# Performance work log

Hardware: AMD Instinct MI355X
Metric: run time of the kernel (lower is better)

The kernel has to match this reference:

```python
import jax, jax.numpy as jnp
import numpy as np
from jax.ops import segment_sum, segment_max

N_NODES = 100000
N_EDGES = 1600000


def _glorot(key, shape):
    fan_in, fan_out = shape[0], shape[-1]
    lim = np.sqrt(6.0 / (fan_in + fan_out))
    return jax.random.uniform(key, shape, jnp.float32, -lim, lim)


def setup_inputs() -> dict:
    key = jax.random.key(0)
    ks = jax.random.split(key, 12)
    x = jax.random.normal(ks[0], (N_NODES, 7), jnp.float32)
    edge_index = jax.random.randint(ks[1], (2, N_EDGES), 0, N_NODES, jnp.int64)
    return {
        "x": x,
        "edge_index": edge_index,
        # GCNConv(7, 32)
        "W1": _glorot(ks[2], (7, 32)), "b1": jnp.zeros((32,), jnp.float32),
        # GATConv(32, 64), heads=1
        "W2": _glorot(ks[3], (32, 64)), "a_src2": _glorot(ks[4], (64, 1))[:, 0],
        "a_dst2": _glorot(ks[5], (64, 1))[:, 0], "b2": jnp.zeros((64,), jnp.float32),
        # GCNConv(64, 128)
        "W3": _glorot(ks[6], (64, 128)), "b3": jnp.zeros((128,), jnp.float32),
        # GATConv(128, 2), heads=1
        "W4": _glorot(ks[7], (128, 2)), "a_src4": _glorot(ks[8], (2, 1))[:, 0],
        "a_dst4": _glorot(ks[9], (2, 1))[:, 0], "b4": jnp.zeros((2,), jnp.float32),
    }


def _gcn_conv(x, src, dst, W, b):
    # x' = W x; symmetric normalization with self-loops already in (src, dst)
    h = x @ W
    deg = segment_sum(jnp.ones_like(dst, dtype=h.dtype), dst, num_segments=N_NODES)
    dinv = jnp.where(deg > 0, jax.lax.rsqrt(deg), 0.0)
    norm = dinv[src] * dinv[dst]            # [E]
    msg = norm[:, None] * h[src]            # [E, C]
    return segment_sum(msg, dst, num_segments=N_NODES) + b


def _gat_conv(x, src, dst, W, a_src, a_dst, b, slope=0.2):
    h = x @ W                               # [N, C]
    alpha_src = h @ a_src                   # [N]
    alpha_dst = h @ a_dst                   # [N]
    e = alpha_src[src] + alpha_dst[dst]     # [E]
    e = jnp.where(e > 0, e, slope * e)      # leaky_relu
    # numerically-stable softmax over edges grouped by destination node
    m = segment_max(e, dst, num_segments=N_NODES)
    ex = jnp.exp(e - m[dst])
    denom = segment_sum(ex, dst, num_segments=N_NODES)
    w = ex / (denom[dst] + 1e-16)           # [E]
    out = segment_sum(w[:, None] * h[src], dst, num_segments=N_NODES)
    return out + b


def reference(x, edge_index, W1, b1, W2, a_src2, a_dst2, b2, W3, b3, W4, a_src4, a_dst4, b4):
    # add self-loops once (PyG does it per layer; identical edge set each time)
    loop = jnp.arange(N_NODES, dtype=edge_index.dtype)
    src = jnp.concatenate([edge_index[0], loop])
    dst = jnp.concatenate([edge_index[1], loop])

    h = _gcn_conv(x, src, dst, W1, b1)
    h = jax.nn.relu(h)
    h = _gat_conv(h, src, dst, W2, a_src2, a_dst2, b2)
    h = jax.nn.relu(h)
    h = _gcn_conv(h, src, dst, W3, b3)
    h = jax.nn.relu(h)
    h = _gat_conv(h, src, dst, W4, a_src4, a_dst4, b4)
    return jax.nn.log_softmax(h, axis=1)
```

## Files before the change

kernel.cpp:

```cpp
#include <hip/hip_runtime.h>
#include <hip/hip_bf16.h>

#define NN 100000
#define NE 1600000
#define NT (NN + NE)
#define NBKT 256
#define BSZ 391
#define BCAP 10240

typedef unsigned int u32;
typedef unsigned short u16;

static __device__ __forceinline__ int clampN(int s) {
    return ((unsigned)s < (unsigned)NN) ? s : 0;
}
static __device__ __forceinline__ int ld_src(const int* ei, int is32, int e) {
    return is32 ? ei[e] : ei[2 * e];
}
static __device__ __forceinline__ int ld_dst(const int* ei, int is32, int e) {
    return is32 ? ei[NE + e] : ei[2 * NE + 2 * e];
}
static __device__ __forceinline__ float2 b2x2(u32 u) {
    float2 r;
    r.x = __uint_as_float((u & 0xffffu) << 16);
    r.y = __uint_as_float(u & 0xffff0000u);
    return r;
}
static __device__ __forceinline__ u16 f2bs(float f) {
    union { __hip_bfloat16 b; u16 u; } cv;
    cv.b = __float2bfloat16(f);
    return cv.u;
}
static __device__ __forceinline__ u32 pack2(float x, float y) {
    return ((u32)f2bs(y) << 16) | (u32)f2bs(x);
}
static __device__ __forceinline__ float lrelu_c(float e) {
    e = (e > 0.f) ? e : 0.2f * e;
    return fminf(e, 60.f);
}

#define FMA4(acc, s, v) { acc.x += (s)*(v).x; acc.y += (s)*(v).y; \
                          acc.z += (s)*(v).z; acc.w += (s)*(v).w; }


__global__ void __launch_bounds__(256) k_init(const float* __restrict__ W2,
                                              const float* __restrict__ a2s,
                                              const float* __restrict__ a2d,
                                              const int* __restrict__ ei,
                                              float* __restrict__ va2,
                                              float* __restrict__ vd2,
                                              int* __restrict__ flag,
                                              int* __restrict__ gcur) {
    if (blockIdx.x == 0) {
        if (threadIdx.x == 0) flag[0] = 0;
        __syncthreads();
        int nz = 0;
        for (int i = threadIdx.x; i < 4096; i += 256) nz |= ei[2 * i + 1];
        if (nz) atomicOr(flag, 1);
        if (threadIdx.x < NBKT) gcur[threadIdx.x] = 0;
    } else if (threadIdx.x < 64) {
        int t = threadIdx.x;
        if (t < 32) {
            float a = 0.f;
            for (int c = 0; c < 64; c++) a += W2[t * 64 + c] * a2s[c];
            va2[t] = a;
        } else {
            int k = t - 32;
            float a = 0.f;
            for (int c = 0; c < 64; c++) a += W2[k * 64 + c] * a2d[c];
            vd2[k] = a;
        }
    }
}


__global__ void __launch_bounds__(256) k_binA(const int* __restrict__ ei,
                                              const int* __restrict__ flag,
                                              int* __restrict__ gcur,
                                              u32* __restrict__ staging) {
    __shared__ int hist[NBKT];
    __shared__ int gbase[NBKT];
    __shared__ int cnt2[NBKT];
    int tid = threadIdx.x;
    if (tid < NBKT) hist[tid] = 0;
    __syncthreads();

    int base = blockIdx.x * 4096;
    int is32 = flag[0];
    int d[16], s[16];
    #pragma unroll
    for (int i = 0; i < 16; i++) {
        int e = base + i * 256 + tid;
        d[i] = -1;
        if (e < NE) {
            int dd = ld_dst(ei, is32, e);
            if ((unsigned)dd < (unsigned)NN) { d[i] = dd; s[i] = clampN(ld_src(ei, is32, e)); }
        } else if (e < NT) {
            d[i] = e - NE; s[i] = e - NE;
        }
        if (d[i] >= 0) atomicAdd(&hist[d[i] / BSZ], 1);
    }
    __syncthreads();
    if (tid < NBKT) {
        int c = hist[tid];
        gbase[tid] = c ? atomicAdd(&gcur[tid], c) : 0;
        cnt2[tid] = 0;
    }
    __syncthreads();
    #pragma unroll
    for (int i = 0; i < 16; i++) {
        if (d[i] >= 0) {
            int b = d[i] / BSZ;
            int pos = gbase[b] + atomicAdd(&cnt2[b], 1);
            if (pos < BCAP)
                staging[(size_t)b * BCAP + pos] =
                    ((unsigned)(d[i] - b * BSZ) << 17) | (unsigned)s[i];
        }
    }
}

__global__ void __launch_bounds__(256) k_histscan(const u32* __restrict__ staging,
                                                  const int* __restrict__ gcur,
                                                  const float* __restrict__ x,
                                                  u32* __restrict__ xpb,
                                                  int* __restrict__ rowptr,
                                                  int* __restrict__ deg,
                                                  int* __restrict__ part) {
    __shared__ int h[512];
    __shared__ int sm[256];
    int b = blockIdx.x, tid = threadIdx.x;
    h[tid] = 0; h[tid + 256] = 0;
    __syncthreads();
    int cnt = min(gcur[b], BCAP);
    const u32* st = staging + (size_t)b * BCAP;
    for (int i = tid; i < cnt; i += 256)
        atomicAdd(&h[st[i] >> 17], 1);
    __syncthreads();
    int h0 = h[2 * tid], h1 = h[2 * tid + 1];
    int pair = h0 + h1;
    sm[tid] = pair;
    __syncthreads();
    for (int off = 1; off < 256; off <<= 1) {
        int t = (tid >= off) ? sm[tid - off] : 0;
        __syncthreads();
        sm[tid] += t;
        __syncthreads();
    }
    int excl = sm[tid] - pair;
    int g0 = b * BSZ + 2 * tid;
    if (2 * tid < BSZ && g0 < NN) { rowptr[g0] = excl; deg[g0] = h0; }
    int g1 = g0 + 1;
    if (2 * tid + 1 < BSZ && g1 < NN) { rowptr[g1] = excl + h0; deg[g1] = h1; }
    if (tid == 255) part[b] = sm[255];

    for (int i = b * 256 + tid; i < NN * 4; i += NBKT * 256) {
        int n = i >> 2, c2 = i & 3;
        float f0 = x[n * 7 + 2 * c2];
        float f1 = (2 * c2 + 1 < 7) ? x[n * 7 + 2 * c2 + 1] : 0.f;
        xpb[i] = pack2(f0, f1);
    }
}

__global__ void __launch_bounds__(256) k_scat(const u32* __restrict__ staging,
                                              const int* __restrict__ gcur,
                                              const int* __restrict__ part,
                                              int* __restrict__ rowptr,
                                              const int* __restrict__ deg,
                                              float* __restrict__ dinv,
                                              int* __restrict__ col) {
    __shared__ int sm[256];
    __shared__ int cur[BSZ];
    int b = blockIdx.x, tid = threadIdx.x;
    int v = part[tid];
    sm[tid] = v;
    __syncthreads();
    for (int off = 1; off < 256; off <<= 1) {
        int t = (tid >= off) ? sm[tid - off] : 0;
        __syncthreads();
        sm[tid] += t;
        __syncthreads();
    }
    int pb = (b > 0) ? sm[b - 1] : 0;
    if (b == 0 && tid == 0) rowptr[NN] = NT;
    for (int l = tid; l < BSZ; l += 256) {
        int g = b * BSZ + l;
        if (g < NN) {
            int r = rowptr[g] + pb;
            rowptr[g] = r;
            cur[l] = r;
            int d = deg[g];
            dinv[g] = rsqrtf((float)(d > 0 ? d : 1));
        } else cur[l] = 0;
    }
    __syncthreads();
    int cnt = min(gcur[b], BCAP);
    const u32* st = staging + (size_t)b * BCAP;
    for (int i = tid; i < cnt; i += 256) {
        u32 w = st[i];
        int l = w >> 17;
        int s = w & 0x1FFFF;
        int p = atomicAdd(&cur[l], 1);
        if ((unsigned)p < (unsigned)NT) col[p] = s;
    }
}


__global__ void __launch_bounds__(256) k_l1(const u32* __restrict__ xpb,
                                            const int* __restrict__ rowptr,
                                            const int* __restrict__ col,
                                            const float* __restrict__ dinv,
                                            const float* __restrict__ W1,
                                            const float* __restrict__ b1,
                                            const float* __restrict__ va2,
                                            const float* __restrict__ vd2,
                                            u32* __restrict__ O1b,
                                            float* __restrict__ as_,
                                            float* __restrict__ ad_) {
    __shared__ float sW1[7 * 32];
    __shared__ float sb1[32], sva[32], svd[32];
    __shared__ float sT1[64 * 8];
    if (threadIdx.x < 224) sW1[threadIdx.x] = W1[threadIdx.x];
    else {
        int c = threadIdx.x - 224;
        sb1[c] = b1[c]; sva[c] = va2[c]; svd[c] = vd2[c];
    }
    __syncthreads();

    int node_l = threadIdx.x >> 2;
    int lane = threadIdx.x & 3;
    int slot = lane >> 1;
    int ck = lane & 1;
    int n = blockIdx.x * 64 + node_l;
    if (n >= NN) return;
    {
        int beg = rowptr[n], end = rowptr[n + 1];
        float a0 = 0.f, a1 = 0.f, a2 = 0.f, a3 = 0.f;
        #pragma unroll 2
        for (int e = beg + slot; e < end; e += 2) {
            int s = clampN(col[e]);
            float w = dinv[s];
            uint2 u = *(const uint2*)(xpb + (size_t)s * 4 + ck * 2);
            float2 f0 = b2x2(u.x), f1 = b2x2(u.y);
            a0 += w * f0.x; a1 += w * f0.y; a2 += w * f1.x; a3 += w * f1.y;
        }
        a0 += __shfl_xor(a0, 2, 4); a1 += __shfl_xor(a1, 2, 4);
        a2 += __shfl_xor(a2, 2, 4); a3 += __shfl_xor(a3, 2, 4);
        if (slot == 0) {
            float dn = dinv[n];
            float4 o = {a0 * dn, a1 * dn, a2 * dn, a3 * dn};
            *(float4*)&sT1[node_l * 8 + ck * 4] = o;
        }
    }
    __builtin_amdgcn_wave_barrier();
    int c8 = lane * 8;
    float4 aA = {0,0,0,0}, aB = {0,0,0,0};
    #pragma unroll
    for (int k = 0; k < 7; k++) {
        float t = sT1[node_l * 8 + k];
        float4 wva = *(const float4*)&sW1[k * 32 + c8];
        float4 wvb = *(const float4*)&sW1[k * 32 + c8 + 4];
        FMA4(aA, t, wva);
        FMA4(aB, t, wvb);
    }
    float o0 = fmaxf(aA.x + sb1[c8], 0.f);
    float o1 = fmaxf(aA.y + sb1[c8 + 1], 0.f);
    float o2 = fmaxf(aA.z + sb1[c8 + 2], 0.f);
    float o3 = fmaxf(aA.w + sb1[c8 + 3], 0.f);
    float o4 = fmaxf(aB.x + sb1[c8 + 4], 0.f);
    float o5 = fmaxf(aB.y + sb1[c8 + 5], 0.f);
    float o6 = fmaxf(aB.z + sb1[c8 + 6], 0.f);
    float o7 = fmaxf(aB.w + sb1[c8 + 7], 0.f);
    uint4 pk = {pack2(o0, o1), pack2(o2, o3), pack2(o4, o5), pack2(o6, o7)};
    *(uint4*)(O1b + (size_t)n * 16 + lane * 4) = pk;
    float vs = o0 * sva[c8] + o1 * sva[c8 + 1] + o2 * sva[c8 + 2] + o3 * sva[c8 + 3]
             + o4 * sva[c8 + 4] + o5 * sva[c8 + 5] + o6 * sva[c8 + 6] + o7 * sva[c8 + 7];
    float vd = o0 * svd[c8] + o1 * svd[c8 + 1] + o2 * svd[c8 + 2] + o3 * svd[c8 + 3]
             + o4 * svd[c8 + 4] + o5 * svd[c8 + 5] + o6 * svd[c8 + 6] + o7 * svd[c8 + 7];
    vs += __shfl_xor(vs, 1, 4); vs += __shfl_xor(vs, 2, 4);
    vd += __shfl_xor(vd, 1, 4); vd += __shfl_xor(vd, 2, 4);
    if (lane == 0) { as_[n] = vs; ad_[n] = vd; }
}


__global__ void __launch_bounds__(256) k_l2(const u32* __restrict__ O1b,
                                            const float* __restrict__ as_,
                                            const float* __restrict__ ad_,
                                            const int* __restrict__ rowptr,
                                            const int* __restrict__ col,
                                            const float* __restrict__ W2,
                                            const float* __restrict__ b2,
                                            const float* __restrict__ dinv,
                                            u32* __restrict__ O2b) {
    __shared__ float sW2[32 * 64];
    __shared__ float sT2[32 * 36];
    __shared__ float sb2[64];
    {
        const float4* g = (const float4*)W2;
        float4* s4 = (float4*)sW2;
        s4[threadIdx.x] = g[threadIdx.x];
        s4[threadIdx.x + 256] = g[threadIdx.x + 256];
    }
    if (threadIdx.x < 64) sb2[threadIdx.x] = b2[threadIdx.x];
    __syncthreads();

    int node_l = threadIdx.x >> 3;
    int l8 = threadIdx.x & 7;
    int slot = l8 >> 2;
    int ck = l8 & 3;
    int n = blockIdx.x * 32 + node_l;
    {
        int beg = rowptr[n], end = rowptr[n + 1];
        float adn = ad_[n];
        float den = 0.f;
        float a0=0.f,a1=0.f,a2=0.f,a3=0.f,a4=0.f,a5=0.f,a6=0.f,a7=0.f;
        #pragma unroll 2
        for (int e = beg + slot; e < end; e += 2) {
            int s = clampN(col[e]);
            float p = __expf(lrelu_c(as_[s] + adn));
            den += p;
            uint4 w = *(const uint4*)(O1b + (size_t)s * 16 + ck * 4);
            float2 f0 = b2x2(w.x), f1 = b2x2(w.y), f2 = b2x2(w.z), f3 = b2x2(w.w);
            a0 += p * f0.x; a1 += p * f0.y; a2 += p * f1.x; a3 += p * f1.y;
            a4 += p * f2.x; a5 += p * f2.y; a6 += p * f3.x; a7 += p * f3.y;
        }
        den += __shfl_xor(den, 4, 8);
        a0 += __shfl_xor(a0, 4, 8); a1 += __shfl_xor(a1, 4, 8);
        a2 += __shfl_xor(a2, 4, 8); a3 += __shfl_xor(a3, 4, 8);
        a4 += __shfl_xor(a4, 4, 8); a5 += __shfl_xor(a5, 4, 8);
        a6 += __shfl_xor(a6, 4, 8); a7 += __shfl_xor(a7, 4, 8);
        if (slot == 0) {
            float inv = 1.0f / (den + 1e-16f);
            float4 oA = {a0 * inv, a1 * inv, a2 * inv, a3 * inv};
            float4 oB = {a4 * inv, a5 * inv, a6 * inv, a7 * inv};
            float* dst = &sT2[node_l * 36 + ck * 8];
            *(float4*)dst = oA;
            *(float4*)(dst + 4) = oB;
        }
    }
    __builtin_amdgcn_wave_barrier();

    int grp = threadIdx.x >> 4;
    int l = threadIdx.x & 15;
    int c4 = l * 4;
    int lbase = grp * 2;

    float4 acc0 = {0,0,0,0}, acc1 = {0,0,0,0};
    #pragma unroll
    for (int k4 = 0; k4 < 8; k4++) {
        float4 t0 = *(const float4*)&sT2[(lbase + 0) * 36 + 4 * k4];
        float4 t1 = *(const float4*)&sT2[(lbase + 1) * 36 + 4 * k4];
        #pragma unroll
        for (int j = 0; j < 4; j++) {
            float4 wv = *(const float4*)&sW2[(4 * k4 + j) * 64 + c4];
            FMA4(acc0, ((const float*)&t0)[j], wv);
            FMA4(acc1, ((const float*)&t1)[j], wv);
        }
    }
    float4 bb = *(const float4*)&sb2[c4];
    int n0 = blockIdx.x * 32 + lbase;
    float d0 = dinv[n0], d1 = dinv[n0 + 1];
    {
        float o0 = fmaxf(acc0.x + bb.x, 0.f) * d0;
        float o1 = fmaxf(acc0.y + bb.y, 0.f) * d0;
        float o2 = fmaxf(acc0.z + bb.z, 0.f) * d0;
        float o3 = fmaxf(acc0.w + bb.w, 0.f) * d0;
        uint2 pk = {pack2(o0, o1), pack2(o2, o3)};
        *(uint2*)(O2b + (size_t)n0 * 32 + l * 2) = pk;
    }
    {
        float o0 = fmaxf(acc1.x + bb.x, 0.f) * d1;
        float o1 = fmaxf(acc1.y + bb.y, 0.f) * d1;
        float o2 = fmaxf(acc1.z + bb.z, 0.f) * d1;
        float o3 = fmaxf(acc1.w + bb.w, 0.f) * d1;
        uint2 pk = {pack2(o0, o1), pack2(o2, o3)};
        *(uint2*)(O2b + (size_t)(n0 + 1) * 32 + l * 2) = pk;
    }
}


__global__ void __launch_bounds__(512) k_l3(const u32* __restrict__ O2b,
                                            const int* __restrict__ rowptr,
                                            const int* __restrict__ col,
                                            const float* __restrict__ dinv,
                                            const float* __restrict__ W3,
                                            const float* __restrict__ b3,
                                            const float* __restrict__ W4,
                                            const float* __restrict__ av4s,
                                            const float* __restrict__ av4d,
                                            float4* __restrict__ h4as,
                                            float* __restrict__ ad_) {
    __shared__ float sW3[64 * 128];
    __shared__ float sT3[64 * 68];
    __shared__ float sW4[128 * 2];
    __shared__ float sb3[128];

    {
        const float4* g = (const float4*)W3;
        float4* s4 = (float4*)sW3;
        #pragma unroll
        for (int i = 0; i < 4; i++) s4[threadIdx.x + 512 * i] = g[threadIdx.x + 512 * i];
    }
    if (threadIdx.x < 128) {
        sb3[threadIdx.x] = b3[threadIdx.x];
        sW4[2 * threadIdx.x] = W4[2 * threadIdx.x];
        sW4[2 * threadIdx.x + 1] = W4[2 * threadIdx.x + 1];
    }
    __syncthreads();

    int w = threadIdx.x >> 6;
    int l = threadIdx.x & 63;
    int g8 = l >> 3;
    int row = w * 8 + g8;
    int n = blockIdx.x * 64 + row;
    if (n >= NN) return;

    {
        int slot = (l >> 2) & 1;
        int ck = l & 3;
        int beg = rowptr[n], end = rowptr[n + 1];
        float2 ac[8];
        #pragma unroll
        for (int i = 0; i < 8; i++) { ac[i].x = 0.f; ac[i].y = 0.f; }
        #pragma unroll 2
        for (int e = beg + slot; e < end; e += 2) {
            int s = clampN(col[e]);
            const uint4* rp = (const uint4*)(O2b + (size_t)s * 32 + ck * 8);
            uint4 wa = rp[0];
            uint4 wb = rp[1];
            float2 f;
            f = b2x2(wa.x); ac[0].x += f.x; ac[0].y += f.y;
            f = b2x2(wa.y); ac[1].x += f.x; ac[1].y += f.y;
            f = b2x2(wa.z); ac[2].x += f.x; ac[2].y += f.y;
            f = b2x2(wa.w); ac[3].x += f.x; ac[3].y += f.y;
            f = b2x2(wb.x); ac[4].x += f.x; ac[4].y += f.y;
            f = b2x2(wb.y); ac[5].x += f.x; ac[5].y += f.y;
            f = b2x2(wb.z); ac[6].x += f.x; ac[6].y += f.y;
            f = b2x2(wb.w); ac[7].x += f.x; ac[7].y += f.y;
        }
        #pragma unroll
        for (int i = 0; i < 8; i++) {
            ac[i].x += __shfl_xor(ac[i].x, 4, 8);
            ac[i].y += __shfl_xor(ac[i].y, 4, 8);
        }
        if (slot == 0) {
            float dn = dinv[n];
            float* dst = &sT3[row * 68 + ck * 16];
            float4 o0 = {ac[0].x * dn, ac[0].y * dn, ac[1].x * dn, ac[1].y * dn};
            float4 o1 = {ac[2].x * dn, ac[2].y * dn, ac[3].x * dn, ac[3].y * dn};
            float4 o2 = {ac[4].x * dn, ac[4].y * dn, ac[5].x * dn, ac[5].y * dn};
            float4 o3 = {ac[6].x * dn, ac[6].y * dn, ac[7].x * dn, ac[7].y * dn};
            *(float4*)&dst[0]  = o0;
            *(float4*)&dst[4]  = o1;
            *(float4*)&dst[8]  = o2;
            *(float4*)&dst[12] = o3;
        }
    }
    __builtin_amdgcn_wave_barrier();

    int cl = l & 7;
    const float* trow = &sT3[row * 68];
    float4 acc0 = {0,0,0,0}, acc1 = {0,0,0,0}, acc2 = {0,0,0,0}, acc3 = {0,0,0,0};
    #pragma unroll 4
    for (int k4 = 0; k4 < 16; k4++) {
        float4 t4 = *(const float4*)&trow[k4 * 4];
        #pragma unroll
        for (int j = 0; j < 4; j++) {
            float tj = ((const float*)&t4)[j];
            const float* wr = &sW3[(k4 * 4 + j) * 128 + 4 * cl];
            float4 w0 = *(const float4*)&wr[0];
            float4 w1 = *(const float4*)&wr[32];
            float4 w2 = *(const float4*)&wr[64];
            float4 w3v = *(const float4*)&wr[96];
            FMA4(acc0, tj, w0);
            FMA4(acc1, tj, w1);
            FMA4(acc2, tj, w2);
            FMA4(acc3, tj, w3v);
        }
    }

    float av4s0 = av4s[0], av4s1 = av4s[1];
    float av4d0 = av4d[0], av4d1 = av4d[1];
    float p0 = 0.f, p1 = 0.f;
    #pragma unroll
    for (int q = 0; q < 4; q++) {
        float4 a = (q == 0) ? acc0 : (q == 1) ? acc1 : (q == 2) ? acc2 : acc3;
        int c = 4 * cl + 32 * q;
        float4 bb = *(const float4*)&sb3[c];
        a.x = fmaxf(a.x + bb.x, 0.f);
        a.y = fmaxf(a.y + bb.y, 0.f);
        a.z = fmaxf(a.z + bb.z, 0.f);
        a.w = fmaxf(a.w + bb.w, 0.f);
        p0 += a.x * sW4[2 * c]     + a.y * sW4[2 * (c + 1)]
            + a.z * sW4[2 * (c + 2)] + a.w * sW4[2 * (c + 3)];
        p1 += a.x * sW4[2 * c + 1]     + a.y * sW4[2 * (c + 1) + 1]
            + a.z * sW4[2 * (c + 2) + 1] + a.w * sW4[2 * (c + 3) + 1];
    }
    p0 += __shfl_xor(p0, 1, 8); p0 += __shfl_xor(p0, 2, 8); p0 += __shfl_xor(p0, 4, 8);
    p1 += __shfl_xor(p1, 1, 8); p1 += __shfl_xor(p1, 2, 8); p1 += __shfl_xor(p1, 4, 8);
    if (cl == 0) {
        float asv = p0 * av4s0 + p1 * av4s1;
        float4 pk = {p0, p1, asv, 0.f};
        h4as[n] = pk;
        ad_[n] = p0 * av4d0 + p1 * av4d1;
    }
}


__global__ void k_final(const float4* __restrict__ h4as,
                        const float* __restrict__ ad_, const int* __restrict__ rowptr,
                        const int* __restrict__ col, const float* __restrict__ b,
                        float* __restrict__ out) {
    int gid = blockIdx.x * 256 + threadIdx.x;
    int n = gid >> 2;
    if (n >= NN) return;
    int lsub = gid & 3;
    int beg = rowptr[n], end = rowptr[n + 1];
    float adn = ad_[n];
    float den = 0.f, a0 = 0.f, a1 = 0.f;
    for (int e = beg + lsub; e < end; e += 4) {
        int s = clampN(col[e]);
        float4 h = h4as[s];
        float p = __expf(lrelu_c(h.z + adn));
        den += p;
        a0 += p * h.x;
        a1 += p * h.y;
    }
    den += __shfl_xor(den, 1, 4); den += __shfl_xor(den, 2, 4);
    a0  += __shfl_xor(a0, 1, 4);  a0  += __shfl_xor(a0, 2, 4);
    a1  += __shfl_xor(a1, 1, 4);  a1  += __shfl_xor(a1, 2, 4);
    if (lsub == 0) {
        float inv = 1.0f / (den + 1e-16f);
        float v0 = a0 * inv + b[0];
        float v1 = a1 * inv + b[1];
        float mx = fmaxf(v0, v1);
        float lse = mx + logf(__expf(v0 - mx) + __expf(v1 - mx));
        float2 o = {v0 - lse, v1 - lse};
        *(float2*)(out + n * 2) = o;
    }
}

__global__ void k_sentinel(float* __restrict__ out, float v) {
    int i = blockIdx.x * 256 + threadIdx.x;
    if (i < NN * 2) out[i] = v;
}


extern "C" void kernel_launch(void* const* d_in, const int* in_sizes, int n_in,
                              void* d_out, int out_size, void* d_ws, size_t ws_size,
                              hipStream_t stream) {
    const float* x    = (const float*)d_in[0];
    const int* ei     = (const int*)d_in[1];
    const float* W1   = (const float*)d_in[2];
    const float* b1   = (const float*)d_in[3];
    const float* W2   = (const float*)d_in[4];
    const float* a2s  = (const float*)d_in[5];
    const float* a2d  = (const float*)d_in[6];
    const float* b2   = (const float*)d_in[7];
    const float* W3   = (const float*)d_in[8];
    const float* b3   = (const float*)d_in[9];
    const float* W4   = (const float*)d_in[10];
    const float* a4s  = (const float*)d_in[11];
    const float* a4d  = (const float*)d_in[12];
    const float* b4   = (const float*)d_in[13];
    float* out = (float*)d_out;

    char* base = (char*)d_ws;
    size_t off = 0;
    auto alloc = [&](size_t bytes) {
        char* q = base + off;
        off += (bytes + 255) & ~(size_t)255;
        return q;
    };
    u32* xpb     = (u32*)alloc((size_t)NN * 4 * 4);
    u32* O1b     = (u32*)alloc((size_t)NN * 16 * 4);
    u32* O2b     = (u32*)alloc((size_t)NN * 32 * 4);
    u32* staging = (u32*)alloc((size_t)NBKT * BCAP * 4);
    int* col     = (int*)alloc((size_t)NT * 4);
    int* rowptr  = (int*)alloc((size_t)(NN + 1) * 4);
    int* deg     = (int*)alloc((size_t)NN * 4);
    float* dinv  = (float*)alloc((size_t)NN * 4);
    float* as_   = (float*)alloc((size_t)NN * 4);
    float* ad_   = (float*)alloc((size_t)NN * 4);
    float4* h4as = (float4*)alloc((size_t)NN * 16);
    int* part    = (int*)alloc(512 * 4);
    int* flag    = (int*)alloc(256);
    int* gcur    = (int*)alloc(NBKT * 4);
    float* va2   = (float*)alloc(32 * 4);
    float* vd2   = (float*)alloc(32 * 4);

    float code = 0.f;
    if (off > ws_size)            code = 1000.f + (float)(ws_size >> 20);
    else if (n_in != 14)          code = 2000.f + 10.f * (float)n_in;
    else if (out_size != NN * 2)  code = 3400.f;
    if (code != 0.f) {
        k_sentinel<<<(NN * 2 + 255) / 256, 256, 0, stream>>>(out, code);
        return;
    }

    const int NTILE = (NT + 4095) / 4096;

    k_init<<<2, 256, 0, stream>>>(W2, a2s, a2d, ei, va2, vd2, flag, gcur);
    k_binA<<<NTILE, 256, 0, stream>>>(ei, flag, gcur, staging);
    k_histscan<<<NBKT, 256, 0, stream>>>(staging, gcur, x, xpb, rowptr, deg, part);
    k_scat<<<NBKT, 256, 0, stream>>>(staging, gcur, part, rowptr, deg, dinv, col);

    k_l1<<<(NN + 63) / 64, 256, 0, stream>>>(xpb, rowptr, col, dinv,
                                             W1, b1, va2, vd2, O1b, as_, ad_);
    k_l2<<<NN / 32, 256, 0, stream>>>(O1b, as_, ad_, rowptr, col,
                                      W2, b2, dinv, O2b);
    k_l3<<<(NN + 63) / 64, 512, 0, stream>>>(O2b, rowptr, col, dinv,
                                             W3, b3, W4, a4s, a4d, h4as, ad_);
    k_final<<<NN * 4 / 256 + 1, 256, 0, stream>>>(h4as, ad_, rowptr, col, b4, out);
}
```

Measured before the change: 252.8 us.

## Gather layer-3 rows per 8-lane group and broadcast via shuffles instead of LDS

The layer-3 aggregation now has each 8-lane group walk all neighbor edges serially, with each lane loading a 16-byte slice of the bf16 row, instead of splitting edges across two slots and reducing with shuffles. The aggregated 64-wide row is then passed to the dense W3 matmul through width-8 shuffles rather than being staged in a shared-memory tile, which drops the sT3 buffer and frees LDS. The launch bounds now request 8 blocks per multiprocessor to raise occupancy. In exchange, each edge load is narrower (16 B per lane instead of 32 B), there is less edge-level parallelism within a row, and the matmul now issues extra shuffle instructions.

```diff
diff --git a/kernel.cpp b/kernel.cpp
--- a/kernel.cpp
+++ b/kernel.cpp
@@ -378,19 +378,18 @@
 }
 
 
-__global__ void __launch_bounds__(512) k_l3(const u32* __restrict__ O2b,
-                                            const int* __restrict__ rowptr,
-                                            const int* __restrict__ col,
-                                            const float* __restrict__ dinv,
-                                            const float* __restrict__ W3,
-                                            const float* __restrict__ b3,
-                                            const float* __restrict__ W4,
-                                            const float* __restrict__ av4s,
-                                            const float* __restrict__ av4d,
-                                            float4* __restrict__ h4as,
-                                            float* __restrict__ ad_) {
+__global__ void __launch_bounds__(512, 8) k_l3(const u32* __restrict__ O2b,
+                                               const int* __restrict__ rowptr,
+                                               const int* __restrict__ col,
+                                               const float* __restrict__ dinv,
+                                               const float* __restrict__ W3,
+                                               const float* __restrict__ b3,
+                                               const float* __restrict__ W4,
+                                               const float* __restrict__ av4s,
+                                               const float* __restrict__ av4d,
+                                               float4* __restrict__ h4as,
+                                               float* __restrict__ ad_) {
     __shared__ float sW3[64 * 128];
-    __shared__ float sT3[64 * 68];
     __shared__ float sW4[128 * 2];
     __shared__ float sb3[128];
 
@@ -407,66 +406,44 @@
     }
     __syncthreads();
 
-    int w = threadIdx.x >> 6;
     int l = threadIdx.x & 63;
-    int g8 = l >> 3;
-    int row = w * 8 + g8;
+    int cl = l & 7;
+    int row = (threadIdx.x >> 6) * 8 + (l >> 3);
     int n = blockIdx.x * 64 + row;
     if (n >= NN) return;
 
-    {
-        int slot = (l >> 2) & 1;
-        int ck = l & 3;
+    float4 accA = {0,0,0,0}, accB = {0,0,0,0};
+    {
         int beg = rowptr[n], end = rowptr[n + 1];
-        float2 ac[8];
-        #pragma unroll
-        for (int i = 0; i < 8; i++) { ac[i].x = 0.f; ac[i].y = 0.f; }
-        #pragma unroll 2
-        for (int e = beg + slot; e < end; e += 2) {
+        #pragma unroll 4
+        for (int e = beg; e < end; e++) {
             int s = clampN(col[e]);
-            const uint4* rp = (const uint4*)(O2b + (size_t)s * 32 + ck * 8);
-            uint4 wa = rp[0];
-            uint4 wb = rp[1];
-            float2 f;
-            f = b2x2(wa.x); ac[0].x += f.x; ac[0].y += f.y;
-            f = b2x2(wa.y); ac[1].x += f.x; ac[1].y += f.y;
-            f = b2x2(wa.z); ac[2].x += f.x; ac[2].y += f.y;
-            f = b2x2(wa.w); ac[3].x += f.x; ac[3].y += f.y;
-            f = b2x2(wb.x); ac[4].x += f.x; ac[4].y += f.y;
-            f = b2x2(wb.y); ac[5].x += f.x; ac[5].y += f.y;
-            f = b2x2(wb.z); ac[6].x += f.x; ac[6].y += f.y;
-            f = b2x2(wb.w); ac[7].x += f.x; ac[7].y += f.y;
-        }
-        #pragma unroll
-        for (int i = 0; i < 8; i++) {
-            ac[i].x += __shfl_xor(ac[i].x, 4, 8);
-            ac[i].y += __shfl_xor(ac[i].y, 4, 8);
-        }
-        if (slot == 0) {
-            float dn = dinv[n];
-            float* dst = &sT3[row * 68 + ck * 16];
-            float4 o0 = {ac[0].x * dn, ac[0].y * dn, ac[1].x * dn, ac[1].y * dn};
-            float4 o1 = {ac[2].x * dn, ac[2].y * dn, ac[3].x * dn, ac[3].y * dn};
-            float4 o2 = {ac[4].x * dn, ac[4].y * dn, ac[5].x * dn, ac[5].y * dn};
-            float4 o3 = {ac[6].x * dn, ac[6].y * dn, ac[7].x * dn, ac[7].y * dn};
-            *(float4*)&dst[0]  = o0;
-            *(float4*)&dst[4]  = o1;
-            *(float4*)&dst[8]  = o2;
-            *(float4*)&dst[12] = o3;
-        }
-    }
-    __builtin_amdgcn_wave_barrier();
-
-    int cl = l & 7;
-    const float* trow = &sT3[row * 68];
+            uint4 wd = *(const uint4*)(O2b + (size_t)s * 32 + cl * 4);
+            float2 f0 = b2x2(wd.x), f1 = b2x2(wd.y), f2 = b2x2(wd.z), f3 = b2x2(wd.w);
+            accA.x += f0.x; accA.y += f0.y; accA.z += f1.x; accA.w += f1.y;
+            accB.x += f2.x; accB.y += f2.y; accB.z += f3.x; accB.w += f3.y;
+        }
+        float dn = dinv[n];
+        accA.x *= dn; accA.y *= dn; accA.z *= dn; accA.w *= dn;
+        accB.x *= dn; accB.y *= dn; accB.z *= dn; accB.w *= dn;
+    }
+
     float4 acc0 = {0,0,0,0}, acc1 = {0,0,0,0}, acc2 = {0,0,0,0}, acc3 = {0,0,0,0};
-    #pragma unroll 4
+    #pragma unroll
     for (int k4 = 0; k4 < 16; k4++) {
-        float4 t4 = *(const float4*)&trow[k4 * 4];
+        int src = k4 >> 1;
+        float t0, t1, t2, t3;
+        if (k4 & 1) {
+            t0 = __shfl(accB.x, src, 8); t1 = __shfl(accB.y, src, 8);
+            t2 = __shfl(accB.z, src, 8); t3 = __shfl(accB.w, src, 8);
+        } else {
+            t0 = __shfl(accA.x, src, 8); t1 = __shfl(accA.y, src, 8);
+            t2 = __shfl(accA.z, src, 8); t3 = __shfl(accA.w, src, 8);
+        }
         #pragma unroll
         for (int j = 0; j < 4; j++) {
-            float tj = ((const float*)&t4)[j];
-            const float* wr = &sW3[(k4 * 4 + j) * 128 + 4 * cl];
+            float tj = (j == 0) ? t0 : (j == 1) ? t1 : (j == 2) ? t2 : t3;
+            const float* wr = &sW3[(4 * k4 + j) * 128 + 4 * cl];
             float4 w0 = *(const float4*)&wr[0];
             float4 w1 = *(const float4*)&wr[32];
             float4 w2 = *(const float4*)&wr[64];
```

Measured after the change: 258.4 us. +2.2%, slower.
